# Kernel optimization log

Hardware: AMD Instinct MI355X
Metric: run time of the kernel (lower is better)

The kernel has to match this reference:

```python
import jax, jax.numpy as jnp
import numpy as np

L = 8192      # residues
K = 48        # k_neighbors
NODE = 128    # node_features
EDGE = 128    # edge_features
RBF = 16      # rbf_dim
POS = 16      # pos_embed_dim
AA = 26       # amino-acid alphabet
EPS = 1e-6


def _rbf(D):
    # Gaussian radial basis lift on [2, 22] Angstrom, 16 bins (ProteinMPNN standard)
    mu = jnp.linspace(2.0, 22.0, RBF).astype(D.dtype)
    sigma = (22.0 - 2.0) / RBF
    return jnp.exp(-(((D[..., None] - mu) / sigma) ** 2))


def setup_inputs() -> dict:
    key = jax.random.key(0)
    ks = jax.random.split(key, 8)
    X = jax.random.normal(ks[0], (L, 3), dtype=jnp.float32) * 10.0
    node_h = jax.random.normal(ks[1], (L, NODE), dtype=jnp.float32)
    f_node = jax.random.normal(ks[2], (L, EDGE), dtype=jnp.float32)
    aatype = jax.random.randint(ks[3], (L,), 0, AA, dtype=jnp.int32)
    residue_index = jnp.arange(L, dtype=jnp.int32)
    Wpos = jax.random.normal(ks[4], (16, POS + RBF + 8 + AA), dtype=jnp.float32) * 0.05
    bpos = jnp.zeros((16,), jnp.float32)
    We = jax.random.normal(ks[5], (EDGE, EDGE + 16 + RBF + NODE + NODE), dtype=jnp.float32) * 0.05
    ln_scale = jnp.ones((EDGE,), jnp.float32)
    ln_bias = jnp.zeros((EDGE,), jnp.float32)
    Wproj = jax.random.normal(ks[6], (EDGE, EDGE), dtype=jnp.float32) * 0.05
    bproj = jnp.zeros((EDGE,), jnp.float32)
    return dict(X=X, node_h=node_h, f_node=f_node, Wpos=Wpos, bpos=bpos, We=We,
                ln_scale=ln_scale, ln_bias=ln_bias, Wproj=Wproj, bproj=bproj,
                aatype=aatype, residue_index=residue_index)


def reference(X, node_h, f_node, Wpos, bpos, We, ln_scale, ln_bias, Wproj, bproj,
              aatype, residue_index):
    # pairwise CA distances [L, L] and k nearest neighbors
    diff_all = X[:, None, :] - X[None, :, :]
    D = jnp.sqrt(jnp.sum(diff_all * diff_all, -1) + EPS)
    negk, idx = jax.lax.top_k(-D, K)          # idx: [L, K]
    Dk = -negk                                # [L, K] neighbor distances
    rbf = _rbf(Dk)                            # [L, K, 16]
    # clipped relative sequence position one-hot [L, K, 16]
    off = residue_index[idx] - residue_index[:, None]
    pos_emb = jax.nn.one_hot(jnp.clip(off + POS // 2, 0, POS - 1), POS, dtype=X.dtype)
    # 8 geometric scalars: 5 distance transforms + unit direction vector
    unit = (X[idx] - X[:, None, :]) / (Dk[..., None] + EPS)
    scal = jnp.stack([Dk / 10.0, 1.0 / (1.0 + Dk), jnp.exp(-Dk), jnp.sin(Dk), jnp.cos(Dk)], -1)
    geom = jnp.concatenate([scal, unit], -1)  # [L, K, 8]
    seq_j = jax.nn.one_hot(aatype[idx], AA, dtype=X.dtype)  # [L, K, 26]
    pos_in = jnp.concatenate([pos_emb, rbf, geom, seq_j], -1)  # [L, K, 66]
    e_pos = pos_in @ Wpos.T + bpos            # w_pos: [L, K, 16]
    h_i = jnp.broadcast_to(node_h[:, None, :], (L, K, NODE))
    e_in = jnp.concatenate([f_node[idx], e_pos, rbf, h_i, node_h[idx]], -1)  # [L, K, 416]
    e = e_in @ We.T                           # w_e (no bias): [L, K, EDGE]
    mean = jnp.mean(e, -1, keepdims=True)
    var = jnp.var(e, -1, keepdims=True)
    e = (e - mean) * jax.lax.rsqrt(var + 1e-5) * ln_scale + ln_bias  # norm_edges
    return e @ Wproj.T + bproj                # w_e_proj: [L, K, EDGE]
```

## Files before the change

### kernel.cpp

```cpp
#include <hip/hip_runtime.h>
#include <stdint.h>
#include <math.h>

#define LRES 8192
#define KNB  48
#define ASTR 296

typedef _Float16 half_t;
typedef _Float16 half8 __attribute__((ext_vector_type(8)));
typedef float f4 __attribute__((ext_vector_type(4)));

__global__ void prep_kernel(const float* __restrict__ We, const float* __restrict__ Wproj,
                            const float* __restrict__ Wpos,
                            half_t* __restrict__ WeH, half_t* __restrict__ WpH,
                            float* __restrict__ Wh32, half_t* __restrict__ WposB) {
  int t = blockIdx.x * blockDim.x + threadIdx.x;
  if (t < 128 * 288) {
    int n = t / 288, kp = t % 288;
    int k = kp < 160 ? kp : kp + 128;
    WeH[n * 288 + kp] = (half_t)We[n * 416 + k];
  }
  if (t < 128 * 128) {
    int n = t >> 7, k = t & 127;
    WpH[t] = (half_t)Wproj[t];
    Wh32[k * 128 + n] = We[n * 416 + 160 + k];
  }
  if (t < 512) {
    int p = t >> 5, k = t & 31;
    float v = (k < 8) ? Wpos[p * 66 + 32 + k] : ((k < 16) ? 0.0f : Wpos[p * 66 + k]);
    WposB[t] = (half_t)v;
  }
}

__global__ __launch_bounds__(256) void hbias_kernel(const float* __restrict__ node_h,
                                                    const float* __restrict__ Wh32,
                                                    float* __restrict__ hb) {
  __shared__ float hrow[4][128];
  const int i0 = blockIdx.x * 4;
  const int t = threadIdx.x;
  for (int u = t; u < 512; u += 256) hrow[u >> 7][u & 127] = node_h[(size_t)i0 * 128 + u];
  __syncthreads();
  const int n = t & 127, g = t >> 7;
  float s0 = 0.f, s1 = 0.f;
#pragma unroll 8
  for (int cc = 0; cc < 128; ++cc) {
    float w = Wh32[cc * 128 + n];
    s0 = fmaf(w, hrow[g][cc], s0);
    s1 = fmaf(w, hrow[g + 2][cc], s1);
  }
  hb[(size_t)(i0 + g) * 128 + n] = s0;
  hb[(size_t)(i0 + g + 2) * 128 + n] = s1;
}

__global__ __launch_bounds__(256) void knn_kernel(const float* __restrict__ X,
                                                  int* __restrict__ out_idx,
                                                  float* __restrict__ out_D) {
  __shared__ unsigned hist[1024];
  __shared__ unsigned psum[256];
  __shared__ double candD[256];
  __shared__ int candJ[256];
  __shared__ unsigned cnt;
  __shared__ int bstar_s;
  __shared__ unsigned cexp_s;
  const int i = blockIdx.x;
  const int tid = threadIdx.x;
  const float xi = X[i * 3 + 0], yi = X[i * 3 + 1], zi = X[i * 3 + 2];
  for (int b = tid; b < 1024; b += 256) hist[b] = 0u;
  if (tid == 0) cnt = 0u;
  __syncthreads();
  unsigned binp[16];
#pragma unroll
  for (int it = 0; it < 8; ++it) {
    int jb = (tid + it * 256) * 4;
    const float* xp = X + (size_t)jb * 3;
    f4 r0 = *(const f4*)(xp);
    f4 r1 = *(const f4*)(xp + 4);
    f4 r2 = *(const f4*)(xp + 8);
    float px[4] = {r0[0], r0[3], r1[2], r2[1]};
    float py[4] = {r0[1], r1[0], r1[3], r2[2]};
    float pz[4] = {r0[2], r1[1], r2[0], r2[3]};
#pragma unroll
    for (int q = 0; q < 4; ++q) {
      float dx = px[q] - xi, dy = py[q] - yi, dz = pz[q] - zi;
      float D = sqrtf(dx * dx + dy * dy + dz * dz + 1e-6f);
      int b = (int)(D * 4.0f); if (b > 1023) b = 1023;
      int idx = it * 4 + q;
      if (idx & 1) binp[idx >> 1] |= (unsigned)b << 16; else binp[idx >> 1] = (unsigned)b;
      atomicAdd(&hist[b], 1u);
    }
  }
  __syncthreads();
  unsigned s4 = hist[tid * 4 + 0] + hist[tid * 4 + 1] + hist[tid * 4 + 2] + hist[tid * 4 + 3];
  psum[tid] = s4;
  __syncthreads();
  if (tid == 0) {
    unsigned run = 0; int g = 0;
    while (g < 255 && run + psum[g] < KNB) { run += psum[g]; ++g; }
    int b = g * 4;
    while (b < g * 4 + 3 && run + hist[b] < KNB) { run += hist[b]; ++b; }
    bstar_s = b;
    unsigned tot = run + hist[b];
    if (b < 1023) tot += hist[b + 1];
    cexp_s = tot;
  }
  __syncthreads();
  int bthr = bstar_s + 1; if (bthr > 1023) bthr = 1023;
  const unsigned cexp = cexp_s;
  const double xid = (double)xi, yid = (double)yi, zid = (double)zi;
  {
    unsigned cmask = 0u;
#pragma unroll
    for (int idx = 0; idx < 32; ++idx) {
      int b = (int)((binp[idx >> 1] >> ((idx & 1) * 16)) & 0xFFFFu);
      if (b <= bthr) cmask |= (1u << idx);
    }
    while (cmask) {
      int k = __builtin_ctz(cmask);
      cmask &= cmask - 1u;
      int j = (tid + (k >> 2) * 256) * 4 + (k & 3);
      unsigned p = atomicAdd(&cnt, 1u);
      if (p < 256u) {
        double ddx = (double)X[j * 3 + 0] - xid;
        double ddy = (double)X[j * 3 + 1] - yid;
        double ddz = (double)X[j * 3 + 2] - zid;
        candD[p] = sqrt(ddx * ddx + ddy * ddy + ddz * ddz + 1e-6);
        candJ[p] = j;
      }
    }
  }
  __syncthreads();
  unsigned n = cnt;
  if (cexp <= 64u) {
    if (tid < 64) {
      double d = (tid < (int)n) ? candD[tid] : INFINITY;
      int j = (tid < (int)n) ? candJ[tid] : 0x7FFFFFFF;
#pragma unroll
      for (int size = 2; size <= 64; size <<= 1) {
#pragma unroll
        for (int stride = 32; stride > 0; stride >>= 1) {
          if (stride >= size) continue;
          double dp = __shfl_xor(d, stride, 64);
          int jp = __shfl_xor(j, stride, 64);
          bool up = ((tid & size) == 0);
          bool lower = ((tid & stride) == 0);
          bool mine_gt = (d > dp) || (d == dp && j > jp);
          bool part_gt = (dp > d) || (dp == d && jp > j);
          bool keep = lower ? (mine_gt != up) : (part_gt != up);
          d = keep ? d : dp;
          j = keep ? j : jp;
        }
      }
      if (tid < KNB) {
        out_idx[(size_t)i * KNB + tid] = j;
        out_D[(size_t)i * KNB + tid] = (float)d;
      }
    }
    return;
  }
  if (tid >= (int)n) { candD[tid] = INFINITY; candJ[tid] = 0x7FFFFFFF; }
  __syncthreads();
  for (unsigned size = 2; size <= 256; size <<= 1) {
    for (unsigned stride = size >> 1; stride > 0; stride >>= 1) {
      unsigned partner = (unsigned)tid ^ stride;
      if (partner > (unsigned)tid) {
        double da = candD[tid], db = candD[partner];
        int ja = candJ[tid], jb = candJ[partner];
        bool agtb = (da > db) || (da == db && ja > jb);
        bool asc = ((tid & size) == 0);
        if (agtb == asc) {
          candD[tid] = db; candJ[tid] = jb;
          candD[partner] = da; candJ[partner] = ja;
        }
      }
      __syncthreads();
    }
  }
  if (tid < KNB) {
    out_idx[(size_t)i * KNB + tid] = candJ[tid];
    out_D[(size_t)i * KNB + tid] = (float)candD[tid];
  }
}

__global__ __launch_bounds__(256, 4) void edge_kernel(
    const float* __restrict__ X, const float* __restrict__ node_h,
    const float* __restrict__ f_node, const float* __restrict__ Wpos,
    const float* __restrict__ bpos, const float* __restrict__ ln_scale,
    const float* __restrict__ ln_bias, const float* __restrict__ bproj,
    const int* __restrict__ aatype, const int* __restrict__ residue_index,
    const int* __restrict__ ws_idx, const float* __restrict__ ws_D,
    const half_t* __restrict__ WeH, const half_t* __restrict__ WpH,
    const half_t* __restrict__ WposB, const float* __restrict__ hbAll,
    float* __restrict__ out) {
  __shared__ __align__(16) half_t Ald[48 * ASTR];
  __shared__ float poolW[1056];
  __shared__ float hbias[128], lnsL[128], lnbL[128], bprojL[128];
  __shared__ float bposL[16], DkL[48];
  __shared__ int jL[48], pidxL[48], aaL[48];

  float* redS  = poolW;
  float* meanL = poolW + 384;
  float* rstdL = poolW + 432;

  const int i = blockIdx.x;
  const int tid = threadIdx.x;
  const int w = tid >> 6;
  const int lane = tid & 63;
  const int lm = lane & 15;
  const int quad = lane >> 4;
  const int quad8 = quad * 8;
  const int n0 = w * 32 + lm;

  if (tid < 128) {
    lnsL[tid] = ln_scale[tid];
    lnbL[tid] = ln_bias[tid];
    bprojL[tid] = bproj[tid];
    hbias[tid] = hbAll[(size_t)i * 128 + tid];
  }
  for (int t = tid; t < 1056; t += 256) poolW[t] = Wpos[t];
  if (tid < 16) bposL[tid] = bpos[tid];
  const float xi = X[i * 3 + 0], yi = X[i * 3 + 1], zi = X[i * 3 + 2];
  if (tid < KNB) {
    int e = tid;
    int j = ws_idx[(size_t)i * KNB + e];
    float Dk = ws_D[(size_t)i * KNB + e];
    jL[e] = j; DkL[e] = Dk;
    float xj = X[j * 3 + 0], yj = X[j * 3 + 1], zj = X[j * 3 + 2];
    float inv = 1.0f / (Dk + 1e-6f);
    half_t* gr = Ald + e * ASTR + 128;
    gr[0] = (half_t)(Dk / 10.0f);
    gr[1] = (half_t)(1.0f / (1.0f + Dk));
    gr[2] = (half_t)expf(-Dk);
    gr[3] = (half_t)sinf(Dk);
    gr[4] = (half_t)cosf(Dk);
    gr[5] = (half_t)((xj - xi) * inv);
    gr[6] = (half_t)((yj - yi) * inv);
    gr[7] = (half_t)((zj - zi) * inv);
    *(uint2*)(gr + 8)  = (uint2){0u, 0u};
    *(uint2*)(gr + 12) = (uint2){0u, 0u};
    int off = residue_index[j] - residue_index[i] + 8;
    off = off < 0 ? 0 : (off > 15 ? 15 : off);
    pidxL[e] = off;
    aaL[e] = aatype[j];
  }
  __syncthreads();

  for (int t = tid; t < KNB * 16; t += 256) {
    int e = t >> 4, m = t & 15;
    float z = (DkL[e] - (2.0f + (float)m * (20.0f / 15.0f))) * 0.8f;
    Ald[e * ASTR + 144 + m] = (half_t)expf(-z * z);
  }
  {
    const int c4 = lane & 31;
    const int sel = lane >> 5;
#pragma unroll
    for (int it = 0; it < 12; ++it) {
      int e = it * 4 + w;
      size_t j = (size_t)jL[e];
      const float* src = (sel ? node_h : f_node) + j * 128 + 4 * c4;
      f4 v = *(const f4*)src;
      union { uint2 u; half_t h[4]; } p;
      p.h[0] = (half_t)v[0]; p.h[1] = (half_t)v[1];
      p.h[2] = (half_t)v[2]; p.h[3] = (half_t)v[3];
      *(uint2*)(Ald + e * ASTR + sel * 160 + 4 * c4) = p.u;
    }
  }
  half8 bregA[9], bregB[9];
#pragma unroll
  for (int ks = 0; ks < 9; ++ks) {
    bregA[ks] = *(const half8*)(WeH + (size_t)n0 * 288 + ks * 32 + quad8);
    bregB[ks] = *(const half8*)(WeH + (size_t)(n0 + 16) * 288 + ks * 32 + quad8);
  }
  __syncthreads();

  if (w < 3) {
    half8 a = *(const half8*)(Ald + (w * 16 + lm) * ASTR + 128 + quad8);
    half8 bp = *(const half8*)(WposB + lm * 32 + quad8);
    f4 z = {};
    f4 ep = __builtin_amdgcn_mfma_f32_16x16x32_f16(a, bp, z, 0, 0, 0);
    const float* wp = poolW + lm * 66;
    float bb = bposL[lm];
#pragma unroll
    for (int r = 0; r < 4; ++r) {
      int m = w * 16 + quad * 4 + r;
      float s = ep[r] + bb + wp[pidxL[m]] + wp[40 + aaL[m]];
      Ald[m * ASTR + 128 + lm] = (half_t)s;
    }
  }
  __syncthreads();

  f4 acc[3][2] = {};
#pragma unroll
  for (int ks = 0; ks < 9; ++ks) {
#pragma unroll
    for (int mt = 0; mt < 3; ++mt) {
      half8 a = *(const half8*)(Ald + (mt * 16 + lm) * ASTR + ks * 32 + quad8);
      acc[mt][0] = __builtin_amdgcn_mfma_f32_16x16x32_f16(a, bregA[ks], acc[mt][0], 0, 0, 0);
      acc[mt][1] = __builtin_amdgcn_mfma_f32_16x16x32_f16(a, bregB[ks], acc[mt][1], 0, 0, 0);
    }
  }
  half8 b2A[4], b2B[4];
#pragma unroll
  for (int ks = 0; ks < 4; ++ks) {
    b2A[ks] = *(const half8*)(WpH + (size_t)n0 * 128 + ks * 32 + quad8);
    b2B[ks] = *(const half8*)(WpH + (size_t)(n0 + 16) * 128 + ks * 32 + quad8);
  }

  {
    float hb0 = hbias[n0], hb1 = hbias[n0 + 16];
#pragma unroll
    for (int mt = 0; mt < 3; ++mt)
#pragma unroll
      for (int r = 0; r < 4; ++r) { acc[mt][0][r] += hb0; acc[mt][1][r] += hb1; }
  }
#pragma unroll
  for (int mt = 0; mt < 3; ++mt)
#pragma unroll
    for (int r = 0; r < 4; ++r) {
      float e0 = acc[mt][0][r], e1 = acc[mt][1][r];
      float sv = e0 + e1;
      float qv = e0 * e0 + e1 * e1;
#pragma unroll
      for (int m = 1; m < 16; m <<= 1) {
        sv += __shfl_xor(sv, m, 16);
        qv += __shfl_xor(qv, m, 16);
      }
      if (lm == 0) {
        int row = mt * 16 + quad * 4 + r;
        redS[row * 8 + w * 2 + 0] = sv;
        redS[row * 8 + w * 2 + 1] = qv;
      }
    }
  __syncthreads();
  if (tid < KNB) {
    float s = redS[tid * 8 + 0] + redS[tid * 8 + 2] + redS[tid * 8 + 4] + redS[tid * 8 + 6];
    float q = redS[tid * 8 + 1] + redS[tid * 8 + 3] + redS[tid * 8 + 5] + redS[tid * 8 + 7];
    float m = s * (1.0f / 128.0f);
    float var = q * (1.0f / 128.0f) - m * m;
    meanL[tid] = m;
    rstdL[tid] = rsqrtf(var + 1e-5f);
  }
  __syncthreads();

#pragma unroll
  for (int mt = 0; mt < 3; ++mt)
#pragma unroll
    for (int nt = 0; nt < 2; ++nt) {
      int n = n0 + nt * 16;
      float ls = lnsL[n], lb = lnbL[n];
#pragma unroll
      for (int r = 0; r < 4; ++r) {
        int m = mt * 16 + quad * 4 + r;
        float e = (acc[mt][nt][r] - meanL[m]) * rstdL[m] * ls + lb;
        Ald[m * ASTR + n] = (half_t)e;
      }
    }
  __syncthreads();

  f4 acc2[3][2] = {};
#pragma unroll
  for (int ks = 0; ks < 4; ++ks) {
#pragma unroll
    for (int mt = 0; mt < 3; ++mt) {
      half8 a = *(const half8*)(Ald + (mt * 16 + lm) * ASTR + ks * 32 + quad8);
      acc2[mt][0] = __builtin_amdgcn_mfma_f32_16x16x32_f16(a, b2A[ks], acc2[mt][0], 0, 0, 0);
      acc2[mt][1] = __builtin_amdgcn_mfma_f32_16x16x32_f16(a, b2B[ks], acc2[mt][1], 0, 0, 0);
    }
  }

#pragma unroll
  for (int mt = 0; mt < 3; ++mt)
#pragma unroll
    for (int nt = 0; nt < 2; ++nt) {
      int n = n0 + nt * 16;
      float bp = bprojL[n];
#pragma unroll
      for (int r = 0; r < 4; ++r) {
        int m = mt * 16 + quad * 4 + r;
        out[((size_t)i * KNB + m) * 128 + n] = acc2[mt][nt][r] + bp;
      }
    }
}

extern "C" void kernel_launch(void* const* d_in, const int* in_sizes, int n_in,
                              void* d_out, int out_size, void* d_ws, size_t ws_size,
                              hipStream_t stream) {
  const float* X        = (const float*)d_in[0];
  const float* node_h   = (const float*)d_in[1];
  const float* f_node   = (const float*)d_in[2];
  const float* Wpos     = (const float*)d_in[3];
  const float* bpos     = (const float*)d_in[4];
  const float* We       = (const float*)d_in[5];
  const float* ln_scale = (const float*)d_in[6];
  const float* ln_bias  = (const float*)d_in[7];
  const float* Wproj    = (const float*)d_in[8];
  const float* bproj    = (const float*)d_in[9];
  const int*   aatype   = (const int*)d_in[10];
  const int*   residue_index = (const int*)d_in[11];
  float* out = (float*)d_out;

  char* ws = (char*)d_ws;
  int*    ws_idx = (int*)ws;
  float*  ws_D   = (float*)(ws + 1572864);
  half_t* WeH    = (half_t*)(ws + 3145728);
  half_t* WpH    = (half_t*)(ws + 3219456);
  float*  Wh32   = (float*)(ws + 3252224);
  half_t* WposB  = (half_t*)(ws + 3317760);
  float*  hbAll  = (float*)(ws + 3318784);

  prep_kernel<<<144, 256, 0, stream>>>(We, Wproj, Wpos, WeH, WpH, Wh32, WposB);
  hbias_kernel<<<2048, 256, 0, stream>>>(node_h, Wh32, hbAll);
  knn_kernel<<<LRES, 256, 0, stream>>>(X, ws_idx, ws_D);
  edge_kernel<<<LRES, 256, 0, stream>>>(X, node_h, f_node, Wpos, bpos, ln_scale,
                                        ln_bias, bproj, aatype, residue_index,
                                        ws_idx, ws_D, WeH, WpH, WposB, hbAll, out);
}
```

Measured before the change: 394.0 us.

## Pre-convert gathered features to fp16, shrink kNN histogram, slim edge-kernel shared memory

Adds a kernel that converts f_node and node_h to fp16 once, so the edge kernel gathers half-width rows with 16-byte loads instead of converting fp32 per neighbor. The kNN histogram shrinks to 256 bins and first counts only near bins, with a full-range fallback pass when the cutoff is exceeded. The edge kernel drops several shared-memory arrays, precombines position and amino-acid weight tables with the bias, keeps LN and projection parameters in registers, and raises the occupancy hint to 5 blocks. These changes target gather bandwidth, shared-memory atomics and occupancy, at the cost of an extra conversion pass and coarser distance bins (distances past 64 Å clamp to one bin).

New measurement: 425.8 us. 8.1% more time.

```diff
diff --git a/kernel.cpp b/kernel.cpp
--- a/kernel.cpp
+++ b/kernel.cpp
@@ -5,6 +5,7 @@
 #define LRES 8192
 #define KNB  48
 #define ASTR 296
+#define CUT  64
 
 typedef _Float16 half_t;
 typedef _Float16 half8 __attribute__((ext_vector_type(8)));
@@ -32,6 +33,23 @@
   }
 }
 
+__global__ __launch_bounds__(256) void cvt_kernel(const float* __restrict__ f_node,
+                                                  const float* __restrict__ node_h,
+                                                  half_t* __restrict__ fnH,
+                                                  half_t* __restrict__ nhH) {
+  int g = blockIdx.x * 256 + threadIdx.x;
+  int sel = g >> 17;
+  size_t off = (size_t)(g & 131071) * 8;
+  const float* s = sel ? node_h : f_node;
+  half_t* d = sel ? nhH : fnH;
+  f4 a = *(const f4*)(s + off);
+  f4 b = *(const f4*)(s + off + 4);
+  half8 h;
+#pragma unroll
+  for (int j = 0; j < 4; ++j) { h[j] = (half_t)a[j]; h[4 + j] = (half_t)b[j]; }
+  *(half8*)(d + off) = h;
+}
+
 __global__ __launch_bounds__(256) void hbias_kernel(const float* __restrict__ node_h,
                                                     const float* __restrict__ Wh32,
                                                     float* __restrict__ hb) {
@@ -55,20 +73,20 @@
 __global__ __launch_bounds__(256) void knn_kernel(const float* __restrict__ X,
                                                   int* __restrict__ out_idx,
                                                   float* __restrict__ out_D) {
-  __shared__ unsigned hist[1024];
-  __shared__ unsigned psum[256];
+  __shared__ unsigned hist[256];
   __shared__ double candD[256];
   __shared__ int candJ[256];
   __shared__ unsigned cnt;
   __shared__ int bstar_s;
   __shared__ unsigned cexp_s;
+  __shared__ int needFull_s;
   const int i = blockIdx.x;
   const int tid = threadIdx.x;
   const float xi = X[i * 3 + 0], yi = X[i * 3 + 1], zi = X[i * 3 + 2];
-  for (int b = tid; b < 1024; b += 256) hist[b] = 0u;
+  hist[tid] = 0u;
   if (tid == 0) cnt = 0u;
   __syncthreads();
-  unsigned binp[16];
+  unsigned bpack[8];
 #pragma unroll
   for (int it = 0; it < 8; ++it) {
     int jb = (tid + it * 256) * 4;
@@ -83,35 +101,49 @@
     for (int q = 0; q < 4; ++q) {
       float dx = px[q] - xi, dy = py[q] - yi, dz = pz[q] - zi;
       float D = sqrtf(dx * dx + dy * dy + dz * dz + 1e-6f);
-      int b = (int)(D * 4.0f); if (b > 1023) b = 1023;
+      int b = (int)(D * 4.0f); if (b > 255) b = 255;
       int idx = it * 4 + q;
-      if (idx & 1) binp[idx >> 1] |= (unsigned)b << 16; else binp[idx >> 1] = (unsigned)b;
-      atomicAdd(&hist[b], 1u);
-    }
-  }
-  __syncthreads();
-  unsigned s4 = hist[tid * 4 + 0] + hist[tid * 4 + 1] + hist[tid * 4 + 2] + hist[tid * 4 + 3];
-  psum[tid] = s4;
+      int sh = (idx & 3) * 8;
+      if ((idx & 3) == 0) bpack[idx >> 2] = (unsigned)b; else bpack[idx >> 2] |= (unsigned)b << sh;
+      if (b < CUT) atomicAdd(&hist[b], 1u);
+    }
+  }
   __syncthreads();
   if (tid == 0) {
-    unsigned run = 0; int g = 0;
-    while (g < 255 && run + psum[g] < KNB) { run += psum[g]; ++g; }
-    int b = g * 4;
-    while (b < g * 4 + 3 && run + hist[b] < KNB) { run += hist[b]; ++b; }
+    unsigned run = 0; int b = 0;
+    while (b < 255 && run + hist[b] < KNB) { run += hist[b]; ++b; }
     bstar_s = b;
+    needFull_s = (b >= CUT - 1) ? 1 : 0;
     unsigned tot = run + hist[b];
-    if (b < 1023) tot += hist[b + 1];
+    if (b < 255) tot += hist[b + 1];
     cexp_s = tot;
   }
   __syncthreads();
-  int bthr = bstar_s + 1; if (bthr > 1023) bthr = 1023;
+  if (needFull_s) {
+#pragma unroll
+    for (int idx = 0; idx < 32; ++idx) {
+      int b = (int)((bpack[idx >> 2] >> ((idx & 3) * 8)) & 0xFFu);
+      if (b >= CUT) atomicAdd(&hist[b], 1u);
+    }
+    __syncthreads();
+    if (tid == 0) {
+      unsigned run = 0; int b = 0;
+      while (b < 255 && run + hist[b] < KNB) { run += hist[b]; ++b; }
+      bstar_s = b;
+      unsigned tot = run + hist[b];
+      if (b < 255) tot += hist[b + 1];
+      cexp_s = tot;
+    }
+    __syncthreads();
+  }
+  int bthr = bstar_s + 1; if (bthr > 255) bthr = 255;
   const unsigned cexp = cexp_s;
   const double xid = (double)xi, yid = (double)yi, zid = (double)zi;
   {
     unsigned cmask = 0u;
 #pragma unroll
     for (int idx = 0; idx < 32; ++idx) {
-      int b = (int)((binp[idx >> 1] >> ((idx & 1) * 16)) & 0xFFFFu);
+      int b = (int)((bpack[idx >> 2] >> ((idx & 3) * 8)) & 0xFFu);
       if (b <= bthr) cmask |= (1u << idx);
     }
     while (cmask) {
@@ -181,9 +213,9 @@
   }
 }
 
-__global__ __launch_bounds__(256, 4) void edge_kernel(
-    const float* __restrict__ X, const float* __restrict__ node_h,
-    const float* __restrict__ f_node, const float* __restrict__ Wpos,
+__global__ __launch_bounds__(256, 5) void edge_kernel(
+    const float* __restrict__ X, const half_t* __restrict__ fnH,
+    const half_t* __restrict__ nhH, const float* __restrict__ Wpos,
     const float* __restrict__ bpos, const float* __restrict__ ln_scale,
     const float* __restrict__ ln_bias, const float* __restrict__ bproj,
     const int* __restrict__ aatype, const int* __restrict__ residue_index,
@@ -192,14 +224,15 @@
     const half_t* __restrict__ WposB, const float* __restrict__ hbAll,
     float* __restrict__ out) {
   __shared__ __align__(16) half_t Ald[48 * ASTR];
-  __shared__ float poolW[1056];
-  __shared__ float hbias[128], lnsL[128], lnbL[128], bprojL[128];
-  __shared__ float bposL[16], DkL[48];
+  __shared__ float tabPool[672];
+  __shared__ float DkL[48];
   __shared__ int jL[48], pidxL[48], aaL[48];
 
-  float* redS  = poolW;
-  float* meanL = poolW + 384;
-  float* rstdL = poolW + 432;
+  float* pos_tab = tabPool;
+  float* aa_tab  = tabPool + 256;
+  float* redS    = tabPool;
+  float* meanL   = tabPool + 384;
+  float* rstdL   = tabPool + 432;
 
   const int i = blockIdx.x;
   const int tid = threadIdx.x;
@@ -210,14 +243,14 @@
   const int quad8 = quad * 8;
   const int n0 = w * 32 + lm;
 
-  if (tid < 128) {
-    lnsL[tid] = ln_scale[tid];
-    lnbL[tid] = ln_bias[tid];
-    bprojL[tid] = bproj[tid];
-    hbias[tid] = hbAll[(size_t)i * 128 + tid];
-  }
-  for (int t = tid; t < 1056; t += 256) poolW[t] = Wpos[t];
-  if (tid < 16) bposL[tid] = bpos[tid];
+  {
+    int pp = tid >> 4, p = tid & 15;
+    pos_tab[tid] = Wpos[p * 66 + pp] + bpos[p];
+  }
+  for (int t = tid; t < 416; t += 256) {
+    int a = t >> 4, p = t & 15;
+    aa_tab[t] = Wpos[p * 66 + 40 + a];
+  }
   const float xi = X[i * 3 + 0], yi = X[i * 3 + 1], zi = X[i * 3 + 2];
   if (tid < KNB) {
     int e = tid;
@@ -249,20 +282,13 @@
     float z = (DkL[e] - (2.0f + (float)m * (20.0f / 15.0f))) * 0.8f;
     Ald[e * ASTR + 144 + m] = (half_t)expf(-z * z);
   }
-  {
-    const int c4 = lane & 31;
-    const int sel = lane >> 5;
-#pragma unroll
-    for (int it = 0; it < 12; ++it) {
-      int e = it * 4 + w;
-      size_t j = (size_t)jL[e];
-      const float* src = (sel ? node_h : f_node) + j * 128 + 4 * c4;
-      f4 v = *(const f4*)src;
-      union { uint2 u; half_t h[4]; } p;
-      p.h[0] = (half_t)v[0]; p.h[1] = (half_t)v[1];
-      p.h[2] = (half_t)v[2]; p.h[3] = (half_t)v[3];
-      *(uint2*)(Ald + e * ASTR + sel * 160 + 4 * c4) = p.u;
-    }
+#pragma unroll
+  for (int it = 0; it < 6; ++it) {
+    int cid = tid + it * 256;
+    int e = cid >> 5, r = cid & 31;
+    int sel = r >> 4, c8 = r & 15;
+    const half_t* src = (sel ? nhH : fnH) + (size_t)jL[e] * 128 + c8 * 8;
+    *(half8*)(Ald + e * ASTR + sel * 160 + c8 * 8) = *(const half8*)src;
   }
   half8 bregA[9], bregB[9];
 #pragma unroll
@@ -270,6 +296,8 @@
     bregA[ks] = *(const half8*)(WeH + (size_t)n0 * 288 + ks * 32 + quad8);
     bregB[ks] = *(const half8*)(WeH + (size_t)(n0 + 16) * 288 + ks * 32 + quad8);
   }
+  float hb0 = hbAll[(size_t)i * 128 + n0];
+  float hb1 = hbAll[(size_t)i * 128 + n0 + 16];
   __syncthreads();
 
   if (w < 3) {
@@ -277,12 +305,10 @@
     half8 bp = *(const half8*)(WposB + lm * 32 + quad8);
     f4 z = {};
     f4 ep = __builtin_amdgcn_mfma_f32_16x16x32_f16(a, bp, z, 0, 0, 0);
-    const float* wp = poolW + lm * 66;
-    float bb = bposL[lm];
 #pragma unroll
     for (int r = 0; r < 4; ++r) {
       int m = w * 16 + quad * 4 + r;
-      float s = ep[r] + bb + wp[pidxL[m]] + wp[40 + aaL[m]];
+      float s = ep[r] + pos_tab[pidxL[m] * 16 + lm] + aa_tab[aaL[m] * 16 + lm];
       Ald[m * ASTR + 128 + lm] = (half_t)s;
     }
   }
@@ -304,14 +330,14 @@
     b2A[ks] = *(const half8*)(WpH + (size_t)n0 * 128 + ks * 32 + quad8);
     b2B[ks] = *(const half8*)(WpH + (size_t)(n0 + 16) * 128 + ks * 32 + quad8);
   }
-
-  {
-    float hb0 = hbias[n0], hb1 = hbias[n0 + 16];
-#pragma unroll
-    for (int mt = 0; mt < 3; ++mt)
-#pragma unroll
-      for (int r = 0; r < 4; ++r) { acc[mt][0][r] += hb0; acc[mt][1][r] += hb1; }
-  }
+  float ls0 = ln_scale[n0], ls1 = ln_scale[n0 + 16];
+  float lb0 = ln_bias[n0],  lb1 = ln_bias[n0 + 16];
+  float bp0 = bproj[n0],    bp1 = bproj[n0 + 16];
+
+#pragma unroll
+  for (int mt = 0; mt < 3; ++mt)
+#pragma unroll
+    for (int r = 0; r < 4; ++r) { acc[mt][0][r] += hb0; acc[mt][1][r] += hb1; }
 #pragma unroll
   for (int mt = 0; mt < 3; ++mt)
 #pragma unroll
@@ -346,7 +372,7 @@
 #pragma unroll
     for (int nt = 0; nt < 2; ++nt) {
       int n = n0 + nt * 16;
-      float ls = lnsL[n], lb = lnbL[n];
+      float ls = nt ? ls1 : ls0, lb = nt ? lb1 : lb0;
 #pragma unroll
       for (int r = 0; r < 4; ++r) {
         int m = mt * 16 + quad * 4 + r;
@@ -372,7 +398,7 @@
 #pragma unroll
     for (int nt = 0; nt < 2; ++nt) {
       int n = n0 + nt * 16;
-      float bp = bprojL[n];
+      float bp = nt ? bp1 : bp0;
 #pragma unroll
       for (int r = 0; r < 4; ++r) {
         int m = mt * 16 + quad * 4 + r;
@@ -406,11 +432,14 @@
   float*  Wh32   = (float*)(ws + 3252224);
   half_t* WposB  = (half_t*)(ws + 3317760);
   float*  hbAll  = (float*)(ws + 3318784);
+  half_t* fnH    = (half_t*)(ws + 7513088);
+  half_t* nhH    = (half_t*)(ws + 9610240);
 
   prep_kernel<<<144, 256, 0, stream>>>(We, Wproj, Wpos, WeH, WpH, Wh32, WposB);
+  cvt_kernel<<<1024, 256, 0, stream>>>(f_node, node_h, fnH, nhH);
   hbias_kernel<<<2048, 256, 0, stream>>>(node_h, Wh32, hbAll);
   knn_kernel<<<LRES, 256, 0, stream>>>(X, ws_idx, ws_D);
-  edge_kernel<<<LRES, 256, 0, stream>>>(X, node_h, f_node, Wpos, bpos, ln_scale,
+  edge_kernel<<<LRES, 256, 0, stream>>>(X, fnH, nhH, Wpos, bpos, ln_scale,
                                         ln_bias, bproj, aatype, residue_index,
                                         ws_idx, ws_D, WeH, WpH, WposB, hbAll, out);
 }
```
